# Performance work log

Hardware: AMD Instinct MI355X
Metric: run time of the kernel (lower is better)

Reference implementation:

```python
import jax, jax.numpy as jnp
import numpy as np

N = 50000
E = 800000
DES, TW, NUMP, CATP = 768, 768, 4, 3
EMB = 384
THIRD = EMB // 3  # 128


def _lin(key, fan_in, fan_out):
    k1, k2 = jax.random.split(key)
    bound = 1.0 / np.sqrt(fan_in)
    W = jax.random.uniform(k1, (fan_in, fan_out), jnp.float32, -bound, bound)
    b = jax.random.uniform(k2, (fan_out,), jnp.float32, -bound, bound)
    return W, b


def setup_inputs() -> dict:
    key = jax.random.key(0)
    ks = jax.random.split(key, 16)
    des = jax.random.normal(ks[0], (N, DES), jnp.float32)
    tweet = jax.random.normal(ks[1], (N, TW), jnp.float32)
    num_prop = jax.random.normal(ks[2], (N, NUMP), jnp.float32)
    cat_prop = jax.random.normal(ks[3], (N, CATP), jnp.float32)
    edge_index = jax.random.randint(ks[4], (2, E), 0, N, jnp.int64)
    W_des, b_des = _lin(ks[5], DES, THIRD)
    W_num, b_num = _lin(ks[6], NUMP, THIRD)
    W_cat, b_cat = _lin(ks[7], CATP, THIRD)
    W_in, b_in = _lin(ks[8], EMB, EMB)
    W_g1, b_g1 = _lin(ks[9], EMB, EMB)
    W_g2, b_g2 = _lin(ks[10], EMB, EMB)
    W_o1, b_o1 = _lin(ks[11], EMB, EMB)
    W_o2, b_o2 = _lin(ks[12], EMB, 2)
    return dict(des=des, tweet=tweet, num_prop=num_prop, cat_prop=cat_prop,
                edge_index=edge_index,
                W_des=W_des, b_des=b_des, W_num=W_num, b_num=b_num,
                W_cat=W_cat, b_cat=b_cat, W_in=W_in, b_in=b_in,
                W_g1=W_g1, b_g1=b_g1, W_g2=W_g2, b_g2=b_g2,
                W_o1=W_o1, b_o1=b_o1, W_o2=W_o2, b_o2=b_o2)


def _leaky(x):
    return jax.nn.leaky_relu(x, 0.01)


def _gcn_conv(x, edge_index, W, b):
    # PyG GCNConv: x' = D^{-1/2} (A + I) D^{-1/2} (x W) + b
    src, dst = edge_index[0], edge_index[1]
    x = x @ W  # [N, out]
    n = x.shape[0]
    deg = jax.ops.segment_sum(jnp.ones(src.shape[0], x.dtype), dst, num_segments=n) + 1.0  # self-loop
    dinv = jax.lax.rsqrt(deg)  # deg >= 1
    norm = dinv[src] * dinv[dst]  # [E]
    msg = x[src] * norm[:, None]  # [E, out] gather
    agg = jax.ops.segment_sum(msg, dst, num_segments=n)  # scatter-add
    agg = agg + x * (dinv * dinv)[:, None]  # self-loop contribution
    return agg + b


def reference(des, tweet, num_prop, cat_prop, edge_index,
              W_des, b_des, W_num, b_num, W_cat, b_cat, W_in, b_in,
              W_g1, b_g1, W_g2, b_g2, W_o1, b_o1, W_o2, b_o2):
    # eval mode: dropout is identity
    d = _leaky(des @ W_des + b_des)
    n = _leaky(num_prop @ W_num + b_num)
    c = _leaky(cat_prop @ W_cat + b_cat)
    x = jnp.concatenate((d, n, c), axis=1)  # [N, EMB]
    x = _leaky(x @ W_in + b_in)
    x = _gcn_conv(x, edge_index, W_g1, b_g1)
    x = _gcn_conv(x, edge_index, W_g2, b_g2)
    x = _leaky(x @ W_o1 + b_o1)
    return x @ W_o2 + b_o2  # [N, 2]
```

## Files before the change

### kernel.cpp

```cpp
#include <hip/hip_runtime.h>
#include <hip/hip_bf16.h>
#include <cstdint>

#define NFEAT 384
#define DESK 768
#define THIRD 128

typedef __bf16 bf16x8 __attribute__((ext_vector_type(8)));
typedef unsigned short u16x8 __attribute__((ext_vector_type(8)));
typedef unsigned short u16x4 __attribute__((ext_vector_type(4)));
typedef float f32x16 __attribute__((ext_vector_type(16)));
typedef _Float16 h16x2 __attribute__((ext_vector_type(2)));

__device__ __forceinline__ float leaky(float x) { return x > 0.f ? x : 0.01f * x; }

__device__ __forceinline__ unsigned short bfhi(float x) {
  unsigned int u = __float_as_uint(x);
  u += 0x7fffu + ((u >> 16) & 1u);
  return (unsigned short)(u >> 16);
}
__device__ __forceinline__ float bf2f(unsigned short h) {
  return __uint_as_float(((unsigned int)h) << 16);
}
__device__ __forceinline__ void bsplit(float x, unsigned short& h,
                                       unsigned short& l) {
  h = bfhi(x);
  l = bfhi(x - bf2f(h));
}

#define MFMA(a, b, c) __builtin_amdgcn_mfma_f32_32x32x16_bf16(a, b, c, 0, 0, 0)

template <int AFP32, int EPI, int BM>
__global__ __launch_bounds__(256, 2) void mfma_gemm(
    const float* __restrict__ Af, const unsigned short* __restrict__ Ahi,
    const unsigned short* __restrict__ Alo,
    const unsigned short* __restrict__ BThi,
    const unsigned short* __restrict__ BTlo, _Float16* __restrict__ Ch16,
    unsigned short* __restrict__ Chi, unsigned short* __restrict__ Clo,
    const float* __restrict__ bias, int M, int K, int ldc) {
  __shared__ unsigned short AhiL[4 * BM * 8];
  __shared__ unsigned short AloL[4 * BM * 8];
  __shared__ unsigned short BhiL[4 * 128 * 8];
  __shared__ unsigned short BloL[4 * 128 * 8];
  const int tid = threadIdx.x;
  const int lane = tid & 63;
  const int w = tid >> 6;
  constexpr int MR = BM / 64;
  const int wm = (w >> 1) * (BM / 2);
  const int wn = (w & 1) * 64;
  const int lm = lane & 31, lk = lane >> 5;
  const int m_base = blockIdx.x * BM, n_base = blockIdx.y * 128;

  f32x16 acc[MR][2];
#pragma unroll
  for (int mi = 0; mi < MR; mi++)
#pragma unroll
    for (int nt = 0; nt < 2; nt++)
#pragma unroll
      for (int r = 0; r < 16; r++) acc[mi][nt][r] = 0.f;

  constexpr int AIT_F = BM / 32;
  constexpr int AIT_H = BM / 64;
  float4 pa[AIT_F];
  u16x8 pah[AIT_H], pal[AIT_H];
  u16x8 pbh[2], pbl[2];

  auto loadA = [&](int kt) {
    if (AFP32) {
#pragma unroll
      for (int it = 0; it < AIT_F; it++) {
        int r = (tid >> 3) + it * 32;
        int gr = m_base + r;
        float4 av = make_float4(0.f, 0.f, 0.f, 0.f);
        if (gr < M) av = *(const float4*)&Af[(size_t)gr * K + kt + (tid & 7) * 4];
        pa[it] = av;
      }
    } else {
#pragma unroll
      for (int it = 0; it < AIT_H; it++) {
        int r = (tid >> 2) + it * 64;
        int gr = m_base + r;
        u16x8 vh = {0, 0, 0, 0, 0, 0, 0, 0};
        u16x8 vl = {0, 0, 0, 0, 0, 0, 0, 0};
        if (gr < M) {
          vh = *(const u16x8*)&Ahi[(size_t)gr * K + kt + (tid & 3) * 8];
          vl = *(const u16x8*)&Alo[(size_t)gr * K + kt + (tid & 3) * 8];
        }
        pah[it] = vh;
        pal[it] = vl;
      }
    }
  };
  auto loadB = [&](int kt) {
#pragma unroll
    for (int it = 0; it < 2; it++) {
      int n = (tid >> 2) + it * 64;
      pbh[it] = *(const u16x8*)&BThi[(size_t)(n_base + n) * K + kt + (tid & 3) * 8];
      pbl[it] = *(const u16x8*)&BTlo[(size_t)(n_base + n) * K + kt + (tid & 3) * 8];
    }
  };
  auto storeLDS = [&]() {
    if (AFP32) {
#pragma unroll
      for (int it = 0; it < AIT_F; it++) {
        int r = (tid >> 3) + it * 32;
        int q = tid & 7;
        float4 av = pa[it];
        unsigned short h0, h1, h2, h3, l0, l1, l2, l3;
        bsplit(av.x, h0, l0);
        bsplit(av.y, h1, l1);
        bsplit(av.z, h2, l2);
        bsplit(av.w, h3, l3);
        int base = ((q >> 1) * BM + r) * 8 + (q & 1) * 4;
        u16x4 th;
        th.x = h0; th.y = h1; th.z = h2; th.w = h3;
        u16x4 tl;
        tl.x = l0; tl.y = l1; tl.z = l2; tl.w = l3;
        *(u16x4*)&AhiL[base] = th;
        *(u16x4*)&AloL[base] = tl;
      }
    } else {
#pragma unroll
      for (int it = 0; it < AIT_H; it++) {
        int r = (tid >> 2) + it * 64;
        int kb = tid & 3;
        *(u16x8*)&AhiL[(kb * BM + r) * 8] = pah[it];
        *(u16x8*)&AloL[(kb * BM + r) * 8] = pal[it];
      }
    }
#pragma unroll
    for (int it = 0; it < 2; it++) {
      int n = (tid >> 2) + it * 64;
      int kb = tid & 3;
      *(u16x8*)&BhiL[(kb * 128 + n) * 8] = pbh[it];
      *(u16x8*)&BloL[(kb * 128 + n) * 8] = pbl[it];
    }
  };

  loadA(0);
  loadB(0);
  for (int kt = 0; kt < K; kt += 32) {
    storeLDS();
    __syncthreads();
    if (kt + 32 < K) {
      loadA(kt + 32);
      loadB(kt + 32);
    }
#pragma unroll
    for (int ks = 0; ks < 2; ks++) {
      int kb = 2 * ks + lk;
      bf16x8 ah[MR], al[MR];
#pragma unroll
      for (int mi = 0; mi < MR; mi++) {
        ah[mi] = __builtin_bit_cast(
            bf16x8, *(const u16x8*)&AhiL[(kb * BM + wm + mi * 32 + lm) * 8]);
        al[mi] = __builtin_bit_cast(
            bf16x8, *(const u16x8*)&AloL[(kb * BM + wm + mi * 32 + lm) * 8]);
      }
      bf16x8 bh0 = __builtin_bit_cast(
          bf16x8, *(const u16x8*)&BhiL[(kb * 128 + wn + lm) * 8]);
      bf16x8 bh1 = __builtin_bit_cast(
          bf16x8, *(const u16x8*)&BhiL[(kb * 128 + wn + 32 + lm) * 8]);
      bf16x8 bl0 = __builtin_bit_cast(
          bf16x8, *(const u16x8*)&BloL[(kb * 128 + wn + lm) * 8]);
      bf16x8 bl1 = __builtin_bit_cast(
          bf16x8, *(const u16x8*)&BloL[(kb * 128 + wn + 32 + lm) * 8]);
#pragma unroll
      for (int mi = 0; mi < MR; mi++) {
        acc[mi][0] = MFMA(ah[mi], bh0, acc[mi][0]);
        acc[mi][1] = MFMA(ah[mi], bh1, acc[mi][1]);
        acc[mi][0] = MFMA(ah[mi], bl0, acc[mi][0]);
        acc[mi][1] = MFMA(ah[mi], bl1, acc[mi][1]);
        acc[mi][0] = MFMA(al[mi], bh0, acc[mi][0]);
        acc[mi][1] = MFMA(al[mi], bh1, acc[mi][1]);
      }
    }
    __syncthreads();
  }
  const int colb = n_base + wn;
#pragma unroll
  for (int mi = 0; mi < MR; mi++) {
#pragma unroll
    for (int nt = 0; nt < 2; nt++) {
      f32x16 v = acc[mi][nt];
      int col = colb + nt * 32 + lm;
      float bv = (EPI == 0) ? bias[col] : 0.f;
      int rb = m_base + wm + mi * 32 + 4 * lk;
#pragma unroll
      for (int rg = 0; rg < 16; rg++) {
        int row = rb + (rg & 3) + 8 * (rg >> 2);
        if (row < M) {
          float x = v[rg];
          if (EPI == 0) {
            x = leaky(x + bv);
            unsigned short h, l;
            bsplit(x, h, l);
            Chi[(size_t)row * ldc + col] = h;
            Clo[(size_t)row * ldc + col] = l;
          } else {
            Ch16[(size_t)row * ldc + col] = (_Float16)x;
          }
        }
      }
    }
  }
}

__global__ __launch_bounds__(256) void split_transpose_b(
    const float* __restrict__ s0, unsigned short* __restrict__ h0,
    unsigned short* __restrict__ l0, const float* __restrict__ s1,
    unsigned short* __restrict__ h1, unsigned short* __restrict__ l1,
    const float* __restrict__ s2, unsigned short* __restrict__ h2,
    unsigned short* __restrict__ l2) {
  int z = blockIdx.z;
  const float* src = z == 0 ? s0 : (z == 1 ? s1 : s2);
  unsigned short* dsthi = z == 0 ? h0 : (z == 1 ? h1 : h2);
  unsigned short* dstlo = z == 0 ? l0 : (z == 1 ? l1 : l2);
  int R = z == 0 ? 768 : 384;
  int C = z == 0 ? 128 : 384;
  int c0 = blockIdx.x * 32, r0 = blockIdx.y * 32;
  if (c0 >= C || r0 >= R) return;
  __shared__ float tile[32][33];
  int tx = threadIdx.x & 31, ty = threadIdx.x >> 5;
#pragma unroll
  for (int i = 0; i < 4; i++)
    tile[ty + i * 8][tx] = src[(size_t)(r0 + ty + i * 8) * C + c0 + tx];
  __syncthreads();
#pragma unroll
  for (int i = 0; i < 4; i++) {
    int c = c0 + ty + i * 8, r = r0 + tx;
    float v = tile[tx][ty + i * 8];
    unsigned short h, l;
    bsplit(v, h, l);
    dsthi[(size_t)c * R + r] = h;
    dstlo[(size_t)c * R + r] = l;
  }
}

__global__ __launch_bounds__(256) void gemm384(const float* __restrict__ A,
                                               const float* __restrict__ B,
                                               float* __restrict__ C) {
  __shared__ float As[16][68];
  __shared__ float Bs[16][64];
  const int tid = threadIdx.x;
  const int mb = blockIdx.x * 64;
  const int nb = blockIdx.y * 64;
  float acc[4][4] = {};
  const int arow = tid >> 2, akq = tid & 3;
  const int brow = tid >> 4, bc4 = tid & 15;
  const int m0 = (tid >> 4) * 4, n0 = (tid & 15) * 4;
  for (int kk = 0; kk < 384; kk += 16) {
    float4 av = *(const float4*)&A[(mb + arow) * 384 + kk + akq * 4];
    As[akq * 4 + 0][arow] = av.x;
    As[akq * 4 + 1][arow] = av.y;
    As[akq * 4 + 2][arow] = av.z;
    As[akq * 4 + 3][arow] = av.w;
    *(float4*)&Bs[brow][bc4 * 4] =
        *(const float4*)&B[(kk + brow) * 384 + nb + bc4 * 4];
    __syncthreads();
#pragma unroll
    for (int k = 0; k < 16; k++) {
      float4 a4 = *(const float4*)&As[k][m0];
      float4 b4 = *(const float4*)&Bs[k][n0];
      float a[4] = {a4.x, a4.y, a4.z, a4.w};
      float b[4] = {b4.x, b4.y, b4.z, b4.w};
#pragma unroll
      for (int i = 0; i < 4; i++)
#pragma unroll
        for (int j = 0; j < 4; j++) acc[i][j] = fmaf(a[i], b[j], acc[i][j]);
    }
    __syncthreads();
  }
#pragma unroll
  for (int i = 0; i < 4; i++)
#pragma unroll
    for (int j = 0; j < 4; j++)
      C[(mb + m0 + i) * 384 + nb + n0 + j] = acc[i][j];
}

__global__ void uv_kernel(const float* __restrict__ T1,
                          const float* __restrict__ W_o1,
                          const float* __restrict__ b_g1,
                          const float* __restrict__ b_g2,
                          const float* __restrict__ b_o1, float* __restrict__ u,
                          float* __restrict__ v) {
  int j = blockIdx.x * blockDim.x + threadIdx.x;
  if (j < 384) {
    float su = 0.f, sv = 0.f;
    for (int k = 0; k < 384; k++) {
      su = fmaf(T1[k * 384 + j], b_g1[k], su);
      sv = fmaf(W_o1[k * 384 + j], b_g2[k], sv);
    }
    u[j] = su;
    v[j] = sv + b_o1[j];
  }
}

__global__ __launch_bounds__(256) void numcat_kernel(
    const float* __restrict__ num, const float* __restrict__ cat,
    const float* __restrict__ Wn, const float* __restrict__ bn,
    const float* __restrict__ Wc, const float* __restrict__ bc,
    unsigned short* __restrict__ x0hi, unsigned short* __restrict__ x0lo,
    int N) {
  int c = threadIdx.x;
  for (int i = blockIdx.x; i < N; i += gridDim.x) {
    float val;
    if (c < 128) {
      val = bn[c];
      val = fmaf(num[i * 4 + 0], Wn[0 * 128 + c], val);
      val = fmaf(num[i * 4 + 1], Wn[1 * 128 + c], val);
      val = fmaf(num[i * 4 + 2], Wn[2 * 128 + c], val);
      val = fmaf(num[i * 4 + 3], Wn[3 * 128 + c], val);
    } else {
      int cc = c - 128;
      val = bc[cc];
      val = fmaf(cat[i * 3 + 0], Wc[0 * 128 + cc], val);
      val = fmaf(cat[i * 3 + 1], Wc[1 * 128 + cc], val);
      val = fmaf(cat[i * 3 + 2], Wc[2 * 128 + cc], val);
    }
    val = leaky(val);
    unsigned short h, l;
    bsplit(val, h, l);
    size_t o = (size_t)i * NFEAT + 128 + c;
    x0hi[o] = h;
    x0lo[o] = l;
  }
}

__global__ void count_kernel(const int* __restrict__ dst, int* __restrict__ deg,
                             int E) {
  int e = blockIdx.x * blockDim.x + threadIdx.x;
  if (e < E) atomicAdd(&deg[dst[e]], 1);
}

__global__ void scan_reduce(const int* __restrict__ deg,
                            int* __restrict__ partial, int N) {
  __shared__ int sm[512];
  int i = blockIdx.x * 512 + threadIdx.x;
  sm[threadIdx.x] = (i < N) ? deg[i] : 0;
  __syncthreads();
  for (int off = 256; off; off >>= 1) {
    if (threadIdx.x < off) sm[threadIdx.x] += sm[threadIdx.x + off];
    __syncthreads();
  }
  if (threadIdx.x == 0) partial[blockIdx.x] = sm[0];
}

__global__ void scan_top(int* partial, int nb) {
  if (threadIdx.x == 0 && blockIdx.x == 0) {
    int run = 0;
    for (int b = 0; b < nb; b++) {
      int t = partial[b];
      partial[b] = run;
      run += t;
    }
  }
}

__global__ void scan_down(const int* __restrict__ deg,
                          const int* __restrict__ partial,
                          int* __restrict__ offsets, int* __restrict__ cursor,
                          float* __restrict__ dinv, int N, int E) {
  __shared__ int sm[512];
  int t = threadIdx.x;
  int i = blockIdx.x * 512 + t;
  int val = (i < N) ? deg[i] : 0;
  sm[t] = val;
  __syncthreads();
  for (int off = 1; off < 512; off <<= 1) {
    int add = (t >= off) ? sm[t - off] : 0;
    __syncthreads();
    sm[t] += add;
    __syncthreads();
  }
  if (i < N) {
    int ex = partial[blockIdx.x] + sm[t] - val;
    offsets[i] = ex;
    cursor[i] = ex;
    dinv[i] = 1.0f / sqrtf((float)val + 1.0f);
  }
  if (i == 0) offsets[N] = E;
}

__global__ void fill_kernel(const int* __restrict__ src,
                            const int* __restrict__ dst,
                            int* __restrict__ cursor,
                            int* __restrict__ csr_off,
                            float* __restrict__ csr_w,
                            const float* __restrict__ dinv, int E) {
  int e = blockIdx.x * blockDim.x + threadIdx.x;
  if (e < E) {
    int s = src[e], d = dst[e];
    int slot = atomicAdd(&cursor[d], 1);
    csr_off[slot] = s * NFEAT;
    csr_w[slot] = dinv[s] * dinv[d];
  }
}

template <int WRITE_S, int FINAL>
__global__ __launch_bounds__(192) void agg_kernel(
    const _Float16* __restrict__ xin, _Float16* __restrict__ xout,
    const int* __restrict__ offsets, const int* __restrict__ csr_off,
    const float* __restrict__ csr_w, const float* __restrict__ dinv,
    float* __restrict__ sout, const float* __restrict__ svec,
    const float* __restrict__ uvec, const float* __restrict__ vvec,
    const float* __restrict__ W_o2, const float* __restrict__ b_o2,
    float* __restrict__ out, int N) {
  const int t = threadIdx.x;
  const int ff = 2 * t;
  __shared__ int ssrc[192];
  __shared__ float sw[192];
  __shared__ float red[3][2];
  float u0 = 0.f, u1 = 0.f, vc0 = 0.f, vc1 = 0.f;
  float w00 = 0.f, w01 = 0.f, w10 = 0.f, w11 = 0.f, bo0 = 0.f, bo1 = 0.f;
  if (FINAL) {
    u0 = uvec[ff];
    u1 = uvec[ff + 1];
    vc0 = vvec[ff];
    vc1 = vvec[ff + 1];
    w00 = W_o2[ff * 2 + 0];
    w01 = W_o2[ff * 2 + 1];
    w10 = W_o2[(ff + 1) * 2 + 0];
    w11 = W_o2[(ff + 1) * 2 + 1];
    bo0 = b_o2[0];
    bo1 = b_o2[1];
  }
  for (int i = blockIdx.x; i < N; i += gridDim.x) {
    int beg = offsets[i], end = offsets[i + 1];
    float di = dinv[i];
    float dii = di * di;
    h16x2 xs = *(const h16x2*)&xin[(size_t)i * NFEAT + ff];
    float A0x = dii * (float)xs.x, A0y = dii * (float)xs.y;
    float A1x = 0.f, A1y = 0.f, A2x = 0.f, A2y = 0.f, A3x = 0.f, A3y = 0.f;
    float wsum = dii;
    for (int j0 = beg; j0 < end; j0 += 192) {
      int cnt = min(192, end - j0);
      if (t < cnt) {
        ssrc[t] = csr_off[j0 + t];
        sw[t] = csr_w[j0 + t];
      }
      __syncthreads();
      int j = 0;
      for (; j + 8 <= cnt; j += 8) {
        int o0 = ssrc[j + 0], o1 = ssrc[j + 1], o2 = ssrc[j + 2],
            o3 = ssrc[j + 3];
        int o4 = ssrc[j + 4], o5 = ssrc[j + 5], o6 = ssrc[j + 6],
            o7 = ssrc[j + 7];
        float w0 = sw[j + 0], w1 = sw[j + 1], w2 = sw[j + 2], w3 = sw[j + 3];
        float w4 = sw[j + 4], w5 = sw[j + 5], w6 = sw[j + 6], w7 = sw[j + 7];
        h16x2 v0 = *(const h16x2*)&xin[o0 + ff];
        h16x2 v1 = *(const h16x2*)&xin[o1 + ff];
        h16x2 v2 = *(const h16x2*)&xin[o2 + ff];
        h16x2 v3 = *(const h16x2*)&xin[o3 + ff];
        h16x2 v4 = *(const h16x2*)&xin[o4 + ff];
        h16x2 v5 = *(const h16x2*)&xin[o5 + ff];
        h16x2 v6 = *(const h16x2*)&xin[o6 + ff];
        h16x2 v7 = *(const h16x2*)&xin[o7 + ff];
        A0x = fmaf(w0, (float)v0.x, A0x);
        A0y = fmaf(w0, (float)v0.y, A0y);
        A1x = fmaf(w1, (float)v1.x, A1x);
        A1y = fmaf(w1, (float)v1.y, A1y);
        A2x = fmaf(w2, (float)v2.x, A2x);
        A2y = fmaf(w2, (float)v2.y, A2y);
        A3x = fmaf(w3, (float)v3.x, A3x);
        A3y = fmaf(w3, (float)v3.y, A3y);
        A0x = fmaf(w4, (float)v4.x, A0x);
        A0y = fmaf(w4, (float)v4.y, A0y);
        A1x = fmaf(w5, (float)v5.x, A1x);
        A1y = fmaf(w5, (float)v5.y, A1y);
        A2x = fmaf(w6, (float)v6.x, A2x);
        A2y = fmaf(w6, (float)v6.y, A2y);
        A3x = fmaf(w7, (float)v7.x, A3x);
        A3y = fmaf(w7, (float)v7.y, A3y);
        if (WRITE_S) wsum += ((w0 + w1) + (w2 + w3)) + ((w4 + w5) + (w6 + w7));
      }
      for (; j < cnt; j++) {
        float wj = sw[j];
        h16x2 vj = *(const h16x2*)&xin[ssrc[j] + ff];
        A0x = fmaf(wj, (float)vj.x, A0x);
        A0y = fmaf(wj, (float)vj.y, A0y);
        if (WRITE_S) wsum += wj;
      }
      __syncthreads();
    }
    float ax = (A0x + A1x) + (A2x + A3x);
    float ay = (A0y + A1y) + (A2y + A3y);
    if (!FINAL) {
      h16x2 r;
      r.x = (_Float16)ax;
      r.y = (_Float16)ay;
      *(h16x2*)&xout[(size_t)i * NFEAT + ff] = r;
      if (WRITE_S && t == 0) sout[i] = wsum;
    } else {
      float si = svec[i];
      float q0 = leaky(ax + si * u0 + vc0);
      float q1 = leaky(ay + si * u1 + vc1);
      float c0 = q0 * w00 + q1 * w10;
      float c1 = q0 * w01 + q1 * w11;
#pragma unroll
      for (int off2 = 32; off2; off2 >>= 1) {
        c0 += __shfl_down(c0, off2, 64);
        c1 += __shfl_down(c1, off2, 64);
      }
      int wid = t >> 6, lane2 = t & 63;
      if (lane2 == 0) {
        red[wid][0] = c0;
        red[wid][1] = c1;
      }
      __syncthreads();
      if (t == 0) {
        out[i * 2 + 0] = red[0][0] + red[1][0] + red[2][0] + bo0;
        out[i * 2 + 1] = red[0][1] + red[1][1] + red[2][1] + bo1;
      }
    }
  }
}

extern "C" void kernel_launch(void* const* d_in, const int* in_sizes, int n_in,
                              void* d_out, int out_size, void* d_ws,
                              size_t ws_size, hipStream_t stream) {
  const float* des = (const float*)d_in[0];
  const float* num_prop = (const float*)d_in[2];
  const float* cat_prop = (const float*)d_in[3];
  const int* edge = (const int*)d_in[4];
  const float* W_des = (const float*)d_in[5];
  const float* b_des = (const float*)d_in[6];
  const float* W_num = (const float*)d_in[7];
  const float* b_num = (const float*)d_in[8];
  const float* W_cat = (const float*)d_in[9];
  const float* b_cat = (const float*)d_in[10];
  const float* W_in = (const float*)d_in[11];
  const float* b_in = (const float*)d_in[12];
  const float* W_g1 = (const float*)d_in[13];
  const float* b_g1 = (const float*)d_in[14];
  const float* W_g2 = (const float*)d_in[15];
  const float* b_g2 = (const float*)d_in[16];
  const float* W_o1 = (const float*)d_in[17];
  const float* b_o1 = (const float*)d_in[18];
  const float* W_o2 = (const float*)d_in[19];
  const float* b_o2 = (const float*)d_in[20];
  float* out = (float*)d_out;

  const int N = in_sizes[0] / DESK;
  const int E = in_sizes[4] / 2;
  const int* esrc = edge;
  const int* edst = edge + E;

  char* ws = (char*)d_ws;
  size_t off = 0;
  auto alloc = [&](size_t n) {
    off = (off + 255) & ~(size_t)255;
    size_t o = off;
    off += n;
    return o;
  };
  float* bufA = (float*)(ws + alloc((size_t)N * NFEAT * 4));
  float* bufB = (float*)(ws + alloc((size_t)N * NFEAT * 4));
  int* deg = (int*)(ws + alloc((size_t)N * 4));
  int* offsets = (int*)(ws + alloc((size_t)(N + 1) * 4));
  int* cursor = (int*)(ws + alloc((size_t)N * 4));
  int* partial = (int*)(ws + alloc(1024 * 4));
  float* dinv = (float*)(ws + alloc((size_t)N * 4));
  float* svec = (float*)(ws + alloc((size_t)N * 4));
  int* csr_off = (int*)(ws + alloc((size_t)E * 4));
  float* csr_w = (float*)(ws + alloc((size_t)E * 4));
  float* T1 = (float*)(ws + alloc(384 * 384 * 4));
  float* Mmat = (float*)(ws + alloc(384 * 384 * 4));
  float* uvec = (float*)(ws + alloc(384 * 4));
  float* vvec = (float*)(ws + alloc(384 * 4));
  unsigned short* WdThi = (unsigned short*)(ws + alloc(768 * 128 * 2));
  unsigned short* WdTlo = (unsigned short*)(ws + alloc(768 * 128 * 2));
  unsigned short* WiThi = (unsigned short*)(ws + alloc(384 * 384 * 2));
  unsigned short* WiTlo = (unsigned short*)(ws + alloc(384 * 384 * 2));
  unsigned short* MmThi = (unsigned short*)(ws + alloc(384 * 384 * 2));
  unsigned short* MmTlo = (unsigned short*)(ws + alloc(384 * 384 * 2));
  (void)ws_size;
  (void)n_in;
  (void)out_size;

  unsigned short* x0hi = (unsigned short*)bufA;
  unsigned short* x0lo = x0hi + (size_t)N * NFEAT;
  unsigned short* x1hi = (unsigned short*)bufB;
  unsigned short* x1lo = x1hi + (size_t)N * NFEAT;
  _Float16* yb = (_Float16*)bufA;
  _Float16* w1 = (_Float16*)bufB;

  hipMemsetAsync(deg, 0, (size_t)N * 4, stream);

  dim3 g6(6, 6);
  gemm384<<<g6, 256, 0, stream>>>(W_g2, W_o1, T1);
  gemm384<<<g6, 256, 0, stream>>>(W_g1, T1, Mmat);
  uv_kernel<<<2, 256, 0, stream>>>(T1, W_o1, b_g1, b_g2, b_o1, uvec, vvec);
  split_transpose_b<<<dim3(12, 24, 3), 256, 0, stream>>>(
      W_des, WdThi, WdTlo, W_in, WiThi, WiTlo, Mmat, MmThi, MmTlo);

  const int MT = (N + 127) / 128;
  const int MT64 = (N + 63) / 64;
  mfma_gemm<1, 0, 64><<<dim3(MT64, 1), 256, 0, stream>>>(
      des, nullptr, nullptr, WdThi, WdTlo, nullptr, x0hi, x0lo, b_des, N, DESK,
      NFEAT);
  numcat_kernel<<<1024, 256, 0, stream>>>(num_prop, cat_prop, W_num, b_num,
                                          W_cat, b_cat, x0hi, x0lo, N);
  mfma_gemm<0, 0, 128><<<dim3(MT, 3), 256, 0, stream>>>(
      nullptr, x0hi, x0lo, WiThi, WiTlo, nullptr, x1hi, x1lo, b_in, N, NFEAT,
      NFEAT);
  mfma_gemm<0, 1, 128><<<dim3(MT, 3), 256, 0, stream>>>(
      nullptr, x1hi, x1lo, MmThi, MmTlo, yb, nullptr, nullptr, nullptr, N,
      NFEAT, NFEAT);

  const int EB = (E + 255) / 256;
  count_kernel<<<EB, 256, 0, stream>>>(edst, deg, E);
  const int NB = (N + 511) / 512;
  scan_reduce<<<NB, 512, 0, stream>>>(deg, partial, N);
  scan_top<<<1, 64, 0, stream>>>(partial, NB);
  scan_down<<<NB, 512, 0, stream>>>(deg, partial, offsets, cursor, dinv, N, E);
  fill_kernel<<<EB, 256, 0, stream>>>(esrc, edst, cursor, csr_off, csr_w, dinv,
                                      E);

  agg_kernel<1, 0><<<4096, 192, 0, stream>>>(
      yb, w1, offsets, csr_off, csr_w, dinv, svec, nullptr, nullptr, nullptr,
      nullptr, nullptr, nullptr, N);
  agg_kernel<0, 1><<<4096, 192, 0, stream>>>(
      w1, nullptr, offsets, csr_off, csr_w, dinv, nullptr, svec, uvec, vvec,
      W_o2, b_o2, out, N);
}
```

Before: 911.3 us.

## Double-buffer LDS with three-deep register prefetch and grouped tile raster in GEMM

Restructures the GEMM main loop so that LDS is double-buffered and global loads are prefetched three K-steps ahead into rotating register sets. This allows one sync per step instead of two, and lets the store for the next tile overlap the compute on the current one. It also remaps block indices into groups of 8 M-tiles across the 3 N-tiles, so that A rows are reused in cache when gridDim.y is 3. The extra register sets and doubled LDS can raise register pressure and lower occupancy. The loop also assumes the K-step count is a multiple of 6.

```diff
diff --git a/kernel.cpp b/kernel.cpp
--- a/kernel.cpp
+++ b/kernel.cpp
@@ -38,10 +38,10 @@
     const unsigned short* __restrict__ BTlo, _Float16* __restrict__ Ch16,
     unsigned short* __restrict__ Chi, unsigned short* __restrict__ Clo,
     const float* __restrict__ bias, int M, int K, int ldc) {
-  __shared__ unsigned short AhiL[4 * BM * 8];
-  __shared__ unsigned short AloL[4 * BM * 8];
-  __shared__ unsigned short BhiL[4 * 128 * 8];
-  __shared__ unsigned short BloL[4 * 128 * 8];
+  __shared__ unsigned short AhiL[2][4 * BM * 8];
+  __shared__ unsigned short AloL[2][4 * BM * 8];
+  __shared__ unsigned short BhiL[2][4 * 128 * 8];
+  __shared__ unsigned short BloL[2][4 * 128 * 8];
   const int tid = threadIdx.x;
   const int lane = tid & 63;
   const int w = tid >> 6;
@@ -49,7 +49,24 @@
   const int wm = (w >> 1) * (BM / 2);
   const int wn = (w & 1) * 64;
   const int lm = lane & 31, lk = lane >> 5;
-  const int m_base = blockIdx.x * BM, n_base = blockIdx.y * 128;
+
+  int bx = blockIdx.x, by = blockIdx.y;
+  if (gridDim.y == 3) {
+    int lin = by * gridDim.x + bx;
+    int ng = gridDim.x >> 3;
+    int full = ng * 24;
+    if (lin < full) {
+      int g = lin / 24, x = lin - g * 24;
+      bx = g * 8 + (x & 7);
+      by = x >> 3;
+    } else {
+      int rem = lin - full;
+      int mrem = gridDim.x - (ng << 3);
+      bx = (ng << 3) + rem % mrem;
+      by = rem / mrem;
+    }
+  }
+  const int m_base = bx * BM, n_base = by * 128;
 
   f32x16 acc[MR][2];
 #pragma unroll
@@ -61,11 +78,11 @@
 
   constexpr int AIT_F = BM / 32;
   constexpr int AIT_H = BM / 64;
-  float4 pa[AIT_F];
-  u16x8 pah[AIT_H], pal[AIT_H];
-  u16x8 pbh[2], pbl[2];
-
-  auto loadA = [&](int kt) {
+  float4 pa[3][AIT_F];
+  u16x8 pah[3][AIT_H], pal[3][AIT_H];
+  u16x8 pbh[3][2], pbl[3][2];
+
+  auto loadA = [&](int kt, int s) {
     if (AFP32) {
 #pragma unroll
       for (int it = 0; it < AIT_F; it++) {
@@ -73,7 +90,7 @@
         int gr = m_base + r;
         float4 av = make_float4(0.f, 0.f, 0.f, 0.f);
         if (gr < M) av = *(const float4*)&Af[(size_t)gr * K + kt + (tid & 7) * 4];
-        pa[it] = av;
+        pa[s][it] = av;
       }
     } else {
 #pragma unroll
@@ -86,26 +103,26 @@
           vh = *(const u16x8*)&Ahi[(size_t)gr * K + kt + (tid & 3) * 8];
           vl = *(const u16x8*)&Alo[(size_t)gr * K + kt + (tid & 3) * 8];
         }
-        pah[it] = vh;
-        pal[it] = vl;
+        pah[s][it] = vh;
+        pal[s][it] = vl;
       }
     }
   };
-  auto loadB = [&](int kt) {
+  auto loadB = [&](int kt, int s) {
 #pragma unroll
     for (int it = 0; it < 2; it++) {
       int n = (tid >> 2) + it * 64;
-      pbh[it] = *(const u16x8*)&BThi[(size_t)(n_base + n) * K + kt + (tid & 3) * 8];
-      pbl[it] = *(const u16x8*)&BTlo[(size_t)(n_base + n) * K + kt + (tid & 3) * 8];
+      pbh[s][it] = *(const u16x8*)&BThi[(size_t)(n_base + n) * K + kt + (tid & 3) * 8];
+      pbl[s][it] = *(const u16x8*)&BTlo[(size_t)(n_base + n) * K + kt + (tid & 3) * 8];
     }
   };
-  auto storeLDS = [&]() {
+  auto storeLDS = [&](int s, int b) {
     if (AFP32) {
 #pragma unroll
       for (int it = 0; it < AIT_F; it++) {
         int r = (tid >> 3) + it * 32;
         int q = tid & 7;
-        float4 av = pa[it];
+        float4 av = pa[s][it];
         unsigned short h0, h1, h2, h3, l0, l1, l2, l3;
         bsplit(av.x, h0, l0);
         bsplit(av.y, h1, l1);
@@ -116,36 +133,27 @@
         th.x = h0; th.y = h1; th.z = h2; th.w = h3;
         u16x4 tl;
         tl.x = l0; tl.y = l1; tl.z = l2; tl.w = l3;
-        *(u16x4*)&AhiL[base] = th;
-        *(u16x4*)&AloL[base] = tl;
+        *(u16x4*)&AhiL[b][base] = th;
+        *(u16x4*)&AloL[b][base] = tl;
       }
     } else {
 #pragma unroll
       for (int it = 0; it < AIT_H; it++) {
         int r = (tid >> 2) + it * 64;
         int kb = tid & 3;
-        *(u16x8*)&AhiL[(kb * BM + r) * 8] = pah[it];
-        *(u16x8*)&AloL[(kb * BM + r) * 8] = pal[it];
+        *(u16x8*)&AhiL[b][(kb * BM + r) * 8] = pah[s][it];
+        *(u16x8*)&AloL[b][(kb * BM + r) * 8] = pal[s][it];
       }
     }
 #pragma unroll
     for (int it = 0; it < 2; it++) {
       int n = (tid >> 2) + it * 64;
       int kb = tid & 3;
-      *(u16x8*)&BhiL[(kb * 128 + n) * 8] = pbh[it];
-      *(u16x8*)&BloL[(kb * 128 + n) * 8] = pbl[it];
+      *(u16x8*)&BhiL[b][(kb * 128 + n) * 8] = pbh[s][it];
+      *(u16x8*)&BloL[b][(kb * 128 + n) * 8] = pbl[s][it];
     }
   };
-
-  loadA(0);
-  loadB(0);
-  for (int kt = 0; kt < K; kt += 32) {
-    storeLDS();
-    __syncthreads();
-    if (kt + 32 < K) {
-      loadA(kt + 32);
-      loadB(kt + 32);
-    }
+  auto compute = [&](int b) {
 #pragma unroll
     for (int ks = 0; ks < 2; ks++) {
       int kb = 2 * ks + lk;
@@ -153,18 +161,18 @@
 #pragma unroll
       for (int mi = 0; mi < MR; mi++) {
         ah[mi] = __builtin_bit_cast(
-            bf16x8, *(const u16x8*)&AhiL[(kb * BM + wm + mi * 32 + lm) * 8]);
+            bf16x8, *(const u16x8*)&AhiL[b][(kb * BM + wm + mi * 32 + lm) * 8]);
         al[mi] = __builtin_bit_cast(
-            bf16x8, *(const u16x8*)&AloL[(kb * BM + wm + mi * 32 + lm) * 8]);
+            bf16x8, *(const u16x8*)&AloL[b][(kb * BM + wm + mi * 32 + lm) * 8]);
       }
       bf16x8 bh0 = __builtin_bit_cast(
-          bf16x8, *(const u16x8*)&BhiL[(kb * 128 + wn + lm) * 8]);
+          bf16x8, *(const u16x8*)&BhiL[b][(kb * 128 + wn + lm) * 8]);
       bf16x8 bh1 = __builtin_bit_cast(
-          bf16x8, *(const u16x8*)&BhiL[(kb * 128 + wn + 32 + lm) * 8]);
+          bf16x8, *(const u16x8*)&BhiL[b][(kb * 128 + wn + 32 + lm) * 8]);
       bf16x8 bl0 = __builtin_bit_cast(
-          bf16x8, *(const u16x8*)&BloL[(kb * 128 + wn + lm) * 8]);
+          bf16x8, *(const u16x8*)&BloL[b][(kb * 128 + wn + lm) * 8]);
       bf16x8 bl1 = __builtin_bit_cast(
-          bf16x8, *(const u16x8*)&BloL[(kb * 128 + wn + 32 + lm) * 8]);
+          bf16x8, *(const u16x8*)&BloL[b][(kb * 128 + wn + 32 + lm) * 8]);
 #pragma unroll
       for (int mi = 0; mi < MR; mi++) {
         acc[mi][0] = MFMA(ah[mi], bh0, acc[mi][0]);
@@ -175,8 +183,32 @@
         acc[mi][1] = MFMA(al[mi], bh1, acc[mi][1]);
       }
     }
-    __syncthreads();
-  }
+  };
+
+  loadA(0, 0);
+  loadB(0, 0);
+  loadA(32, 1);
+  loadB(32, 1);
+  loadA(64, 2);
+  loadB(64, 2);
+  storeLDS(0, 0);
+  __syncthreads();
+
+  const int NK = K >> 5;
+  for (int m6 = 0; m6 < NK / 6; m6++) {
+#pragma unroll
+    for (int ph = 0; ph < 6; ph++) {
+      const int i = m6 * 6 + ph;
+      if (i + 1 < NK) storeLDS((ph + 1) % 3, (ph + 1) & 1);
+      if (i + 3 < NK) {
+        loadA((i + 3) << 5, ph % 3);
+        loadB((i + 3) << 5, ph % 3);
+      }
+      compute(ph & 1);
+      __syncthreads();
+    }
+  }
+
   const int colb = n_base + wn;
 #pragma unroll
   for (int mi = 0; mi < MR; mi++) {
```

New measurement: 935.3 us. 1.03x slower.
